# Optimization experiments

Measured on AMD Instinct MI355X. Metric: run time of the kernel, lower is better.

## Reference

```python
import jax, jax.numpy as jnp
import numpy as np

H1, H2, H3 = 32, 64, 64
NODEN = 12
NODES_PER_GRAPH = NODEN + 2  # 14
N = 700000                   # 50000 graphs * 14 nodes
E = 4000000


def setup_inputs() -> dict:
    key = jax.random.key(0)
    ks = jax.random.split(key, 8)
    x = jax.random.normal(ks[0], (N, H1), dtype=jnp.float32)
    edges = jax.random.randint(ks[1], (2, E), 0, N, dtype=jnp.int64)
    W1 = jax.random.normal(ks[2], (H1, H2), dtype=jnp.float32) / np.sqrt(H1).astype(np.float32)
    b1 = jnp.zeros((H2,), jnp.float32)
    W2 = jax.random.normal(ks[3], (H2, H3), dtype=jnp.float32) / np.sqrt(H2).astype(np.float32)
    b2 = jnp.zeros((H3,), jnp.float32)
    Wfc = jax.random.normal(ks[4], (H3 * NODES_PER_GRAPH, 1), dtype=jnp.float32) / np.sqrt(H3 * NODES_PER_GRAPH).astype(np.float32)
    bfc = jnp.zeros((1,), jnp.float32)
    return {"x": x, "edges": edges, "W1": W1, "b1": b1, "W2": W2, "b2": b2, "Wfc": Wfc, "bfc": bfc}


def gcn_conv(x, src, dst, W, b, n):
    # PyG GCNConv: h = X W; add self-loops; norm = deg^-1/2[src]*deg^-1/2[dst]
    h = x @ W  # [N, out]
    ones = jnp.ones(src.shape[0], dtype=h.dtype)
    deg = jax.ops.segment_sum(ones, dst, num_segments=n) + jnp.asarray(1.0, h.dtype)  # +1 self-loop
    dinv = jax.lax.rsqrt(deg)  # deg >= 1 always (self-loop)
    norm = dinv[src] * dinv[dst]  # [E]
    agg = jax.ops.segment_sum(h[src] * norm[:, None], dst, num_segments=n)
    agg = agg + h * (dinv * dinv)[:, None]  # self-loop contribution
    return agg + b


def reference(x, edges, W1, b1, W2, b2, Wfc, bfc):
    src, dst = edges[0], edges[1]
    h = jax.nn.relu(gcn_conv(x, src, dst, W1, b1, N))
    # F.dropout(training=False) is identity in eval mode
    h = jax.nn.relu(gcn_conv(h, src, dst, W2, b2, N))
    h = h.reshape(-1, H3 * NODES_PER_GRAPH)  # [B, 896]
    return h @ Wfc + bfc  # [B, 1]
```

## Files before the change

kernel.cpp:

```cpp
#include <hip/hip_runtime.h>
#include <hip/hip_fp16.h>


typedef _Float16 half8 __attribute__((ext_vector_type(8)));
typedef float float4v __attribute__((ext_vector_type(4)));

#define CHUNK 8192
#define BSH 11
#define BNODES 2048
#define DBINS 64

__global__ __launch_bounds__(256) void fallback_kernel(float* __restrict__ out, int n, float v)
{
  int i = blockIdx.x * 256 + threadIdx.x;
  if (i < n) out[i] = v;
}

__device__ inline int edges_shift(const int* __restrict__ edges)
{
  int orv = edges[1] | edges[3] | edges[5] | edges[7] | edges[9] | edges[11] | edges[13] | edges[15];
  return (orv == 0) ? 1 : 0;
}

__global__ __launch_bounds__(256) void hist2_kernel(
    const int* __restrict__ edges, int E, int N,
    int* __restrict__ cnt, int NBK, int* __restrict__ gtot,
    __half* __restrict__ P, __half* __restrict__ F2)
{
  __shared__ int lh[512];
  int t = threadIdx.x;
  int blk = blockIdx.x;
  if (blk == 0) {
    if (t < 8) ((uint2*)(P + (size_t)N * 32))[t] = make_uint2(0, 0);
    else if (t < 24) ((uint2*)(F2 + (size_t)N * 64))[t - 8] = make_uint2(0, 0);
  }
  for (int b = t; b < NBK; b += 256) lh[b] = 0;
  __syncthreads();
  int sh = edges_shift(edges);
  int base = blk * CHUNK;
#pragma unroll
  for (int k = 0; k < CHUNK / 256; k++) {
    int e = base + k * 256 + t;
    if (e < E) {
      int d = edges[(E + e) << sh];
      if ((unsigned)d < (unsigned)N) atomicAdd(&lh[d >> BSH], 1);
    }
  }
  __syncthreads();
  for (int b = t; b < NBK; b += 256)
    cnt[(size_t)blk * NBK + b] = atomicAdd(&gtot[b], lh[b]);
}

__global__ __launch_bounds__(512) void scan_totals_kernel(
    const int* __restrict__ totals, int NBK,
    int* __restrict__ bstart, int* __restrict__ rowptr, int N)
{
  __shared__ int sm[512];
  int t = threadIdx.x;
  int v = (t < NBK) ? totals[t] : 0;
  sm[t] = v;
  __syncthreads();
  for (int off = 1; off < 512; off <<= 1) {
    int x = 0;
    if (t >= off) x = sm[t - off];
    __syncthreads();
    if (t >= off) sm[t] += x;
    __syncthreads();
  }
  if (t < NBK) bstart[t] = sm[t] - v;
  if (t == 0) { bstart[NBK] = sm[511]; rowptr[N] = sm[511] + N; }
}

__global__ __launch_bounds__(256) void pass3_kernel(
    const int* __restrict__ edges, int E, int N,
    const int* __restrict__ cnt, const int* __restrict__ bstart,
    int* __restrict__ pair, int NBK)
{
  __shared__ int lcur[512];
  int t = threadIdx.x;
  int blk = blockIdx.x;
  for (int b = t; b < NBK; b += 256)
    lcur[b] = bstart[b] + cnt[(size_t)blk * NBK + b];
  __syncthreads();
  int sh = edges_shift(edges);
  int base = blk * CHUNK;
#pragma unroll
  for (int k = 0; k < CHUNK / 256; k++) {
    int e = base + k * 256 + t;
    if (e < E) {
      int s = edges[e << sh];
      int d = edges[(E + e) << sh];
      if ((unsigned)s < (unsigned)N && (unsigned)d < (unsigned)N) {
        int pos = atomicAdd(&lcur[d >> BSH], 1);
        pair[pos] = s | ((d & (BNODES - 1)) << 20);
      }
    }
  }
}

__global__ __launch_bounds__(256) void build_kernel(
    const int* __restrict__ pair, const int* __restrict__ bstart,
    int* __restrict__ rowptr, float* __restrict__ dinv, int* __restrict__ col,
    int* __restrict__ dhist, int N)
{
  __shared__ int hist[BNODES];
  __shared__ int cur[BNODES];
  __shared__ int sc[256];
  __shared__ int lh2[DBINS];
  int b = blockIdx.x;
  int t = threadIdx.x;
  int pbeg = bstart[b], pend = bstart[b + 1];
  int colbase = pbeg + (b << BSH);
  if (t < DBINS) lh2[t] = 0;
#pragma unroll
  for (int i = 0; i < BNODES / 256; i++) {
    int idx = i * 256 + t;
    int row = (b << BSH) + idx;
    hist[idx] = (row < N) ? 1 : 0;
  }
  __syncthreads();
  for (int p = pbeg + t; p < pend; p += 256)
    atomicAdd(&hist[(pair[p] >> 20) & (BNODES - 1)], 1);
  __syncthreads();
  int hv[8];
  int tsum = 0;
#pragma unroll
  for (int i = 0; i < 8; i++) { hv[i] = hist[t * 8 + i]; tsum += hv[i]; }
  sc[t] = tsum;
  __syncthreads();
  for (int off = 1; off < 256; off <<= 1) {
    int x = 0;
    if (t >= off) x = sc[t - off];
    __syncthreads();
    if (t >= off) sc[t] += x;
    __syncthreads();
  }
  int run = sc[t] - tsum;
#pragma unroll
  for (int i = 0; i < 8; i++) {
    int idx = t * 8 + i;
    int rp = colbase + run;
    int row = (b << BSH) + idx;
    if (row < N) {
      rowptr[row] = rp;
      dinv[row] = rsqrtf((float)hv[i]);
      col[rp] = row;
      cur[idx] = rp + 1;
      int bin = hv[i] < DBINS ? hv[i] : DBINS - 1;
      atomicAdd(&lh2[bin], 1);
    } else {
      cur[idx] = rp;
    }
    run += hv[i];
  }
  __syncthreads();
  if (t < DBINS && lh2[t]) atomicAdd(&dhist[t], lh2[t]);
  for (int p = pbeg + t; p < pend; p += 256) {
    int v = pair[p];
    int pos = atomicAdd(&cur[(v >> 20) & (BNODES - 1)], 1);
    col[pos] = v & 0xFFFFF;
  }
}

__global__ __launch_bounds__(256) void deg_place_kernel(
    const int* __restrict__ rowptr, const float* __restrict__ dinv,
    const int* __restrict__ dhist, int* __restrict__ dcnt,
    int* __restrict__ perm, int* __restrict__ iperm,
    int2* __restrict__ rowinfo, float* __restrict__ dinv_p, int N)
{
  __shared__ int bb[DBINS];
  __shared__ int lh[DBINS];
  __shared__ int lbase[DBINS];
  int t = threadIdx.x;
  if (t < DBINS) {
    lh[t] = 0;
    int v = dhist[t];
    int incl = v;
#pragma unroll
    for (int off = 1; off < DBINS; off <<= 1) {
      int x = __shfl_up(incl, off);
      if (t >= off) incl += x;
    }
    bb[t] = incl - v;
  }
  __syncthreads();
  int n = blockIdx.x * 256 + t;
  int b = -1, rbeg = 0, rlen = 0;
  if (n < N) {
    rbeg = rowptr[n];
    rlen = rowptr[n + 1] - rbeg;
    b = rlen < DBINS ? rlen : DBINS - 1;
    atomicAdd(&lh[b], 1);
  }
  __syncthreads();
  if (t < DBINS) lbase[t] = lh[t] ? (bb[t] + atomicAdd(&dcnt[t], lh[t])) : 0;
  __syncthreads();
  if (t < DBINS) lh[t] = lbase[t];
  __syncthreads();
  if (n < N) {
    int pos = atomicAdd(&lh[b], 1);
    perm[pos] = n;
    iperm[n] = pos;
    rowinfo[pos] = make_int2(rbeg, rlen);
    dinv_p[pos] = dinv[n];
  }
}

__global__ __launch_bounds__(256) void prep_kernel(
    int* __restrict__ col, const int* __restrict__ iperm, const int* __restrict__ rowptr,
    const float* __restrict__ X, const int* __restrict__ perm,
    const float* __restrict__ dinv_p, __half* __restrict__ P,
    float* __restrict__ out, const float* __restrict__ bfc, int N, int B)
{
  int idx = blockIdx.x * 256 + threadIdx.x;
  int stride = gridDim.x * 256;
  int total = rowptr[N];
  for (int k = idx; k < total; k += stride) col[k] = iperm[col[k]];
  int totp = N * 4;
  for (int i = idx; i < totp; i += stride) {
    int pos = i >> 2, part = i & 3;
    int node = perm[pos];
    const float4* xp = (const float4*)(X + (size_t)node * 32 + part * 8);
    float dv = dinv_p[pos];
    float4 v0 = xp[0], v1 = xp[1];
    half8 h;
    h[0] = (_Float16)(dv * v0.x); h[1] = (_Float16)(dv * v0.y);
    h[2] = (_Float16)(dv * v0.z); h[3] = (_Float16)(dv * v0.w);
    h[4] = (_Float16)(dv * v1.x); h[5] = (_Float16)(dv * v1.y);
    h[6] = (_Float16)(dv * v1.z); h[7] = (_Float16)(dv * v1.w);
    *(half8*)(P + (size_t)pos * 32 + part * 8) = h;
  }
  for (int i = idx; i < B; i += stride) out[i] = bfc[0];
}

__device__ inline void hacc(uint4 v, __half2* a)
{
  a[0] = __hadd2(a[0], *reinterpret_cast<__half2*>(&v.x));
  a[1] = __hadd2(a[1], *reinterpret_cast<__half2*>(&v.y));
  a[2] = __hadd2(a[2], *reinterpret_cast<__half2*>(&v.z));
  a[3] = __hadd2(a[3], *reinterpret_cast<__half2*>(&v.w));
}

__global__ __launch_bounds__(256) void agg1_pos_kernel(
    const __half* __restrict__ P, const int2* __restrict__ rowinfo,
    const int* __restrict__ col, const float* __restrict__ dinv_p,
    const float* __restrict__ W1, const float* __restrict__ b1,
    __half* __restrict__ U, int ntiles, int ndummy)
{
  int lane = threadIdx.x & 63;
  int n16 = lane & 15;
  int quad = lane >> 4;

  half8 bf[4];
#pragma unroll
  for (int jb = 0; jb < 4; jb++)
#pragma unroll
    for (int i = 0; i < 8; i++)
      bf[jb][i] = (_Float16)W1[(quad * 8 + i) * 64 + jb * 16 + n16];
  float b1j[4];
#pragma unroll
  for (int jb = 0; jb < 4; jb++) b1j[jb] = b1[jb * 16 + n16];

  const uint4* P4 = (const uint4*)P;
  _Float16* Uh = (_Float16*)U;
  int wave = (blockIdx.x * 256 + threadIdx.x) >> 6;
  int nw = (gridDim.x * 256) >> 6;
  for (int tile = wave; tile < ntiles; tile += nw) {
    int ut = __builtin_amdgcn_readfirstlane(tile);
    int base = ut * 16;
    int2 ri = rowinfo[base + n16];
    int rbeg = ri.x, rlen = ri.y;
    float dvown = dinv_p[base + n16];

    __half2 z2 = __float2half2_rn(0.f);
    __half2 aA[4] = {z2, z2, z2, z2};
    __half2 aB[4] = {z2, z2, z2, z2};

    for (int j = 0; __any(j < rlen); j += 8) {
      int c[8];
#pragma unroll
      for (int q = 0; q < 8; q++) {
        int cc = col[rbeg + j + q];
        c[q] = (j + q < rlen) ? cc : ndummy;
      }
      uint4 v[8];
#pragma unroll
      for (int q = 0; q < 8; q++) v[q] = P4[((size_t)c[q] << 2) + quad];
#pragma unroll
      for (int q = 0; q < 8; q += 2) { hacc(v[q], aA); hacc(v[q + 1], aB); }
    }
#pragma unroll
    for (int k = 0; k < 4; k++) aA[k] = __hadd2(aA[k], aB[k]);

    half8 a = *reinterpret_cast<half8*>(aA);
    float4v co[4];
#pragma unroll
    for (int jb = 0; jb < 4; jb++) {
      float4v z = {0.f, 0.f, 0.f, 0.f};
      co[jb] = __builtin_amdgcn_mfma_f32_16x16x32_f16(a, bf[jb], z, 0, 0, 0);
    }
#pragma unroll
    for (int r = 0; r < 4; r++) {
      int pos2 = base + quad * 4 + r;
      float dv = __shfl(dvown, quad * 4 + r);
#pragma unroll
      for (int jb = 0; jb < 4; jb++) {
        float h = dv * co[jb][r] + b1j[jb];
        h = h > 0.f ? h : 0.f;
        Uh[(size_t)pos2 * 64 + jb * 16 + n16] = (_Float16)(dv * h);
      }
    }
  }
}

__global__ __launch_bounds__(256) void mfma_final_fused_kernel(
    const __half* __restrict__ U, const int2* __restrict__ rowinfo,
    const int* __restrict__ col, const float* __restrict__ dinv_p,
    const int* __restrict__ perm,
    const float* __restrict__ W2, const float* __restrict__ b2,
    const float* __restrict__ Wfc, float* __restrict__ out,
    int ntiles, int ndummy)
{
  int lane = threadIdx.x & 63;
  int n16 = lane & 15;
  int quad = lane >> 4;

  half8 bf[4][2];
#pragma unroll
  for (int jb = 0; jb < 4; jb++)
#pragma unroll
    for (int kf = 0; kf < 2; kf++)
#pragma unroll
      for (int i = 0; i < 8; i++)
        bf[jb][kf][i] = (_Float16)W2[(kf * 32 + quad * 8 + i) * 64 + jb * 16 + n16];
  float b2j[4];
#pragma unroll
  for (int jb = 0; jb < 4; jb++) b2j[jb] = b2[jb * 16 + n16];

  const uint4* U4 = (const uint4*)U;
  int wave = (blockIdx.x * 256 + threadIdx.x) >> 6;
  int nw = (gridDim.x * 256) >> 6;
  for (int tile = wave; tile < ntiles; tile += nw) {
    int ut = __builtin_amdgcn_readfirstlane(tile);
    int base = ut * 16;
    int2 ri = rowinfo[base + n16];
    int rbeg = ri.x, rlen = ri.y;
    int node = perm[base + n16];
    float dvown = dinv_p[base + n16];

    __half2 z2 = __float2half2_rn(0.f);
    __half2 aE0[4] = {z2, z2, z2, z2};
    __half2 aE1[4] = {z2, z2, z2, z2};
    __half2 aO0[4] = {z2, z2, z2, z2};
    __half2 aO1[4] = {z2, z2, z2, z2};

    for (int j = 0; __any(j < rlen); j += 4) {
      int c0 = col[rbeg + j];
      int c1 = col[rbeg + j + 1];
      int c2 = col[rbeg + j + 2];
      int c3 = col[rbeg + j + 3];
      c0 = (j < rlen) ? c0 : ndummy;
      c1 = (j + 1 < rlen) ? c1 : ndummy;
      c2 = (j + 2 < rlen) ? c2 : ndummy;
      c3 = (j + 3 < rlen) ? c3 : ndummy;
      uint4 v00 = U4[((size_t)c0 << 3) + quad];
      uint4 v01 = U4[((size_t)c0 << 3) + 4 + quad];
      uint4 v10 = U4[((size_t)c1 << 3) + quad];
      uint4 v11 = U4[((size_t)c1 << 3) + 4 + quad];
      uint4 v20 = U4[((size_t)c2 << 3) + quad];
      uint4 v21 = U4[((size_t)c2 << 3) + 4 + quad];
      uint4 v30 = U4[((size_t)c3 << 3) + quad];
      uint4 v31 = U4[((size_t)c3 << 3) + 4 + quad];
      hacc(v00, aE0); hacc(v01, aE1);
      hacc(v10, aO0); hacc(v11, aO1);
      hacc(v20, aE0); hacc(v21, aE1);
      hacc(v30, aO0); hacc(v31, aO1);
    }
#pragma unroll
    for (int k = 0; k < 4; k++) {
      aE0[k] = __hadd2(aE0[k], aO0[k]);
      aE1[k] = __hadd2(aE1[k], aO1[k]);
    }
    __half2 dv = __half2half2(__float2half_rn(dvown));
#pragma unroll
    for (int j = 0; j < 4; j++) {
      aE0[j] = __hmul2(aE0[j], dv);
      aE1[j] = __hmul2(aE1[j], dv);
    }
    half8 a0 = *reinterpret_cast<half8*>(aE0);
    half8 a1 = *reinterpret_cast<half8*>(aE1);

    int g_r[4], t_r[4];
#pragma unroll
    for (int r = 0; r < 4; r++) {
      int nd = __shfl(node, quad * 4 + r);
      g_r[r] = nd / 14;
      t_r[r] = nd - g_r[r] * 14;
    }
    float pr[4] = {0.f, 0.f, 0.f, 0.f};
#pragma unroll
    for (int jb = 0; jb < 4; jb++) {
      float4v acc = {0.f, 0.f, 0.f, 0.f};
      acc = __builtin_amdgcn_mfma_f32_16x16x32_f16(a0, bf[jb][0], acc, 0, 0, 0);
      acc = __builtin_amdgcn_mfma_f32_16x16x32_f16(a1, bf[jb][1], acc, 0, 0, 0);
      int j = jb * 16 + n16;
#pragma unroll
      for (int r = 0; r < 4; r++) {
        float h = acc[r] + b2j[jb];
        h = h > 0.f ? h : 0.f;
        pr[r] += h * Wfc[t_r[r] * 64 + j];
      }
    }
#pragma unroll
    for (int r = 0; r < 4; r++) {
#pragma unroll
      for (int off = 1; off < 16; off <<= 1) pr[r] += __shfl_xor(pr[r], off);
    }
    if (n16 == 0) {
#pragma unroll
      for (int r = 0; r < 4; r++) atomicAdd(&out[g_r[r]], pr[r]);
    }
  }
}

extern "C" void kernel_launch(void* const* d_in, const int* in_sizes, int n_in,
                              void* d_out, int out_size, void* d_ws, size_t ws_size,
                              hipStream_t stream)
{
  const float* x = (const float*)d_in[0];
  const int* edges = (const int*)d_in[1];
  const float* W1 = (const float*)d_in[2];
  const float* b1 = (const float*)d_in[3];
  const float* W2 = (const float*)d_in[4];
  const float* b2 = (const float*)d_in[5];
  const float* Wfc = (const float*)d_in[6];
  const float* bfc = (const float*)d_in[7];
  float* out = (float*)d_out;
  (void)n_in;

  const int N = in_sizes[0] / 32;
  const int E = in_sizes[1] / 2;
  const int B = out_size;
  const int NBK = (N + BNODES - 1) >> BSH;
  const int NCH = (E + CHUNK - 1) / CHUNK;
  const int NBLK = (N + 255) / 256;

  char* ws = (char*)d_ws;
  size_t off = 0;
  auto alloc = [&](size_t bytes) -> void* {
    void* p = ws + off;
    off += (bytes + 255) & ~(size_t)255;
    return p;
  };
  int* cnt = (int*)alloc((size_t)NCH * NBK * 4);
  int* zbuf = (int*)alloc(((size_t)NBK + 2 * DBINS) * 4);
  int* gtot = zbuf;
  int* dhist = zbuf + NBK;
  int* dcnt = zbuf + NBK + DBINS;
  int* bstart = (int*)alloc(((size_t)NBK + 1) * 4);
  int* col = (int*)alloc(((size_t)E + N + 256) * 4);
  int* rowptr = (int*)alloc(((size_t)N + 1) * 4);
  float* dinv = (float*)alloc((size_t)N * 4);
  int* perm = (int*)alloc((size_t)N * 4);
  int* iperm = (int*)alloc((size_t)N * 4);
  int2* rowinfo = (int2*)alloc((size_t)N * 8);
  float* dinv_p = (float*)alloc((size_t)N * 4);
  __half* P = (__half*)alloc(((size_t)N + 16) * 32 * 2);
  __half* F2 = (__half*)alloc(((size_t)N + 16) * 64 * 2);
  int* pair = (int*)P;

  if (off > ws_size) {
    float v = -(float)(double)(ws_size >> 20);
    fallback_kernel<<<(B + 255) / 256, 256, 0, stream>>>(out, B, v);
    return;
  }

  hipMemsetAsync(zbuf, 0, ((size_t)NBK + 2 * DBINS) * 4, stream);
  hist2_kernel<<<NCH, 256, 0, stream>>>(edges, E, N, cnt, NBK, gtot, P, F2);
  scan_totals_kernel<<<1, 512, 0, stream>>>(gtot, NBK, bstart, rowptr, N);
  pass3_kernel<<<NCH, 256, 0, stream>>>(edges, E, N, cnt, bstart, pair, NBK);
  build_kernel<<<NBK, 256, 0, stream>>>(pair, bstart, rowptr, dinv, col, dhist, N);
  deg_place_kernel<<<NBLK, 256, 0, stream>>>(rowptr, dinv, dhist, dcnt,
                                             perm, iperm, rowinfo, dinv_p, N);
  prep_kernel<<<4096, 256, 0, stream>>>(col, iperm, rowptr, x, perm, dinv_p, P,
                                        out, bfc, N, B);

  int ntiles = (N + 15) / 16;
  agg1_pos_kernel<<<4096, 256, 0, stream>>>(P, rowinfo, col, dinv_p, W1, b1, F2, ntiles, N);
  mfma_final_fused_kernel<<<4096, 256, 0, stream>>>(F2, rowinfo, col, dinv_p, perm, W2, b2, Wfc,
                                                    out, ntiles, N);
}
```

Measured before the change: 562.3 us.

## Build CSR directly in degree-sorted order via global atomics and scatter

```diff
diff --git a/kernel.cpp b/kernel.cpp
--- a/kernel.cpp
+++ b/kernel.cpp
@@ -5,10 +5,7 @@
 typedef _Float16 half8 __attribute__((ext_vector_type(8)));
 typedef float float4v __attribute__((ext_vector_type(4)));
 
-#define CHUNK 8192
-#define BSH 11
-#define BNODES 2048
-#define DBINS 64
+#define DBINS 128
 
 __global__ __launch_bounds__(256) void fallback_kernel(float* __restrict__ out, int n, float v)
 {
@@ -22,200 +19,113 @@
   return (orv == 0) ? 1 : 0;
 }
 
-__global__ __launch_bounds__(256) void hist2_kernel(
-    const int* __restrict__ edges, int E, int N,
-    int* __restrict__ cnt, int NBK, int* __restrict__ gtot,
+__global__ __launch_bounds__(256) void hist_deg_kernel(
+    const int* __restrict__ edges, int E, int N, int* __restrict__ deg,
     __half* __restrict__ P, __half* __restrict__ F2)
 {
-  __shared__ int lh[512];
   int t = threadIdx.x;
-  int blk = blockIdx.x;
-  if (blk == 0) {
+  if (blockIdx.x == 0) {
     if (t < 8) ((uint2*)(P + (size_t)N * 32))[t] = make_uint2(0, 0);
     else if (t < 24) ((uint2*)(F2 + (size_t)N * 64))[t - 8] = make_uint2(0, 0);
   }
-  for (int b = t; b < NBK; b += 256) lh[b] = 0;
-  __syncthreads();
   int sh = edges_shift(edges);
-  int base = blk * CHUNK;
-#pragma unroll
-  for (int k = 0; k < CHUNK / 256; k++) {
-    int e = base + k * 256 + t;
-    if (e < E) {
-      int d = edges[(E + e) << sh];
-      if ((unsigned)d < (unsigned)N) atomicAdd(&lh[d >> BSH], 1);
-    }
-  }
-  __syncthreads();
-  for (int b = t; b < NBK; b += 256)
-    cnt[(size_t)blk * NBK + b] = atomicAdd(&gtot[b], lh[b]);
-}
-
-__global__ __launch_bounds__(512) void scan_totals_kernel(
-    const int* __restrict__ totals, int NBK,
-    int* __restrict__ bstart, int* __restrict__ rowptr, int N)
-{
-  __shared__ int sm[512];
+  int stride = gridDim.x * 256;
+  for (int e = blockIdx.x * 256 + t; e < E; e += stride) {
+    int s = edges[e << sh];
+    int d = edges[(E + e) << sh];
+    if ((unsigned)s < (unsigned)N && (unsigned)d < (unsigned)N)
+      atomicAdd(&deg[d], 1);
+  }
+}
+
+__global__ __launch_bounds__(256) void dbin_hist_kernel(
+    const int* __restrict__ deg, int* __restrict__ dhist, int N)
+{
+  __shared__ int lh[DBINS];
   int t = threadIdx.x;
-  int v = (t < NBK) ? totals[t] : 0;
-  sm[t] = v;
-  __syncthreads();
-  for (int off = 1; off < 512; off <<= 1) {
-    int x = 0;
-    if (t >= off) x = sm[t - off];
+  if (t < DBINS) lh[t] = 0;
+  __syncthreads();
+  int n = blockIdx.x * 256 + t;
+  if (n < N) {
+    int r = deg[n] + 1;
+    int b = r < DBINS ? r : DBINS - 1;
+    atomicAdd(&lh[b], 1);
+  }
+  __syncthreads();
+  if (t < DBINS && lh[t]) atomicAdd(&dhist[t], lh[t]);
+}
+
+__global__ __launch_bounds__(256) void deg_place_kernel(
+    const int* __restrict__ deg, const int* __restrict__ dhist, int* __restrict__ dcnt,
+    int* __restrict__ perm, int* __restrict__ iperm,
+    int2* __restrict__ rowinfo, float* __restrict__ dinv_p,
+    int* __restrict__ col, int N)
+{
+  __shared__ int s1[DBINS], s2[DBINS];
+  __shared__ int pb[DBINS], eb[DBINS];
+  __shared__ int lh[DBINS], lbase[DBINS];
+  int t = threadIdx.x;
+  int hv = 0;
+  if (t < DBINS) { hv = dhist[t]; s1[t] = hv; s2[t] = hv * t; lh[t] = 0; }
+  __syncthreads();
+  for (int off = 1; off < DBINS; off <<= 1) {
+    int a = 0, w = 0;
+    if (t < DBINS && t >= off) { a = s1[t - off]; w = s2[t - off]; }
     __syncthreads();
-    if (t >= off) sm[t] += x;
+    if (t < DBINS && t >= off) { s1[t] += a; s2[t] += w; }
     __syncthreads();
   }
-  if (t < NBK) bstart[t] = sm[t] - v;
-  if (t == 0) { bstart[NBK] = sm[511]; rowptr[N] = sm[511] + N; }
-}
-
-__global__ __launch_bounds__(256) void pass3_kernel(
-    const int* __restrict__ edges, int E, int N,
-    const int* __restrict__ cnt, const int* __restrict__ bstart,
-    int* __restrict__ pair, int NBK)
-{
-  __shared__ int lcur[512];
-  int t = threadIdx.x;
-  int blk = blockIdx.x;
-  for (int b = t; b < NBK; b += 256)
-    lcur[b] = bstart[b] + cnt[(size_t)blk * NBK + b];
-  __syncthreads();
-  int sh = edges_shift(edges);
-  int base = blk * CHUNK;
-#pragma unroll
-  for (int k = 0; k < CHUNK / 256; k++) {
-    int e = base + k * 256 + t;
-    if (e < E) {
-      int s = edges[e << sh];
-      int d = edges[(E + e) << sh];
-      if ((unsigned)s < (unsigned)N && (unsigned)d < (unsigned)N) {
-        int pos = atomicAdd(&lcur[d >> BSH], 1);
-        pair[pos] = s | ((d & (BNODES - 1)) << 20);
-      }
-    }
-  }
-}
-
-__global__ __launch_bounds__(256) void build_kernel(
-    const int* __restrict__ pair, const int* __restrict__ bstart,
-    int* __restrict__ rowptr, float* __restrict__ dinv, int* __restrict__ col,
-    int* __restrict__ dhist, int N)
-{
-  __shared__ int hist[BNODES];
-  __shared__ int cur[BNODES];
-  __shared__ int sc[256];
-  __shared__ int lh2[DBINS];
-  int b = blockIdx.x;
-  int t = threadIdx.x;
-  int pbeg = bstart[b], pend = bstart[b + 1];
-  int colbase = pbeg + (b << BSH);
-  if (t < DBINS) lh2[t] = 0;
-#pragma unroll
-  for (int i = 0; i < BNODES / 256; i++) {
-    int idx = i * 256 + t;
-    int row = (b << BSH) + idx;
-    hist[idx] = (row < N) ? 1 : 0;
-  }
-  __syncthreads();
-  for (int p = pbeg + t; p < pend; p += 256)
-    atomicAdd(&hist[(pair[p] >> 20) & (BNODES - 1)], 1);
-  __syncthreads();
-  int hv[8];
-  int tsum = 0;
-#pragma unroll
-  for (int i = 0; i < 8; i++) { hv[i] = hist[t * 8 + i]; tsum += hv[i]; }
-  sc[t] = tsum;
-  __syncthreads();
-  for (int off = 1; off < 256; off <<= 1) {
-    int x = 0;
-    if (t >= off) x = sc[t - off];
-    __syncthreads();
-    if (t >= off) sc[t] += x;
-    __syncthreads();
-  }
-  int run = sc[t] - tsum;
-#pragma unroll
-  for (int i = 0; i < 8; i++) {
-    int idx = t * 8 + i;
-    int rp = colbase + run;
-    int row = (b << BSH) + idx;
-    if (row < N) {
-      rowptr[row] = rp;
-      dinv[row] = rsqrtf((float)hv[i]);
-      col[rp] = row;
-      cur[idx] = rp + 1;
-      int bin = hv[i] < DBINS ? hv[i] : DBINS - 1;
-      atomicAdd(&lh2[bin], 1);
-    } else {
-      cur[idx] = rp;
-    }
-    run += hv[i];
-  }
-  __syncthreads();
-  if (t < DBINS && lh2[t]) atomicAdd(&dhist[t], lh2[t]);
-  for (int p = pbeg + t; p < pend; p += 256) {
-    int v = pair[p];
-    int pos = atomicAdd(&cur[(v >> 20) & (BNODES - 1)], 1);
-    col[pos] = v & 0xFFFFF;
-  }
-}
-
-__global__ __launch_bounds__(256) void deg_place_kernel(
-    const int* __restrict__ rowptr, const float* __restrict__ dinv,
-    const int* __restrict__ dhist, int* __restrict__ dcnt,
-    int* __restrict__ perm, int* __restrict__ iperm,
-    int2* __restrict__ rowinfo, float* __restrict__ dinv_p, int N)
-{
-  __shared__ int bb[DBINS];
-  __shared__ int lh[DBINS];
-  __shared__ int lbase[DBINS];
-  int t = threadIdx.x;
-  if (t < DBINS) {
-    lh[t] = 0;
-    int v = dhist[t];
-    int incl = v;
-#pragma unroll
-    for (int off = 1; off < DBINS; off <<= 1) {
-      int x = __shfl_up(incl, off);
-      if (t >= off) incl += x;
-    }
-    bb[t] = incl - v;
-  }
+  if (t < DBINS) { pb[t] = s1[t] - hv; eb[t] = s2[t] - hv * t; }
   __syncthreads();
   int n = blockIdx.x * 256 + t;
-  int b = -1, rbeg = 0, rlen = 0;
+  int b = -1, dg = 0;
   if (n < N) {
-    rbeg = rowptr[n];
-    rlen = rowptr[n + 1] - rbeg;
-    b = rlen < DBINS ? rlen : DBINS - 1;
+    dg = deg[n];
+    int r = dg + 1;
+    b = r < DBINS ? r : DBINS - 1;
     atomicAdd(&lh[b], 1);
   }
   __syncthreads();
-  if (t < DBINS) lbase[t] = lh[t] ? (bb[t] + atomicAdd(&dcnt[t], lh[t])) : 0;
+  if (t < DBINS) lbase[t] = lh[t] ? (pb[t] + atomicAdd(&dcnt[t], lh[t])) : 0;
   __syncthreads();
   if (t < DBINS) lh[t] = lbase[t];
   __syncthreads();
   if (n < N) {
     int pos = atomicAdd(&lh[b], 1);
+    int rowbeg = eb[b] + (pos - pb[b]) * b;
     perm[pos] = n;
     iperm[n] = pos;
-    rowinfo[pos] = make_int2(rbeg, rlen);
-    dinv_p[pos] = dinv[n];
+    rowinfo[pos] = make_int2(rowbeg, b);
+    dinv_p[pos] = rsqrtf((float)(dg + 1));
+    col[rowbeg] = pos;
+  }
+}
+
+__global__ __launch_bounds__(256) void scatter_kernel(
+    const int* __restrict__ edges, int E, int N, const int* __restrict__ iperm,
+    const int2* __restrict__ rowinfo, int* __restrict__ ecur, int* __restrict__ col)
+{
+  int sh = edges_shift(edges);
+  int stride = gridDim.x * 256;
+  for (int e = blockIdx.x * 256 + threadIdx.x; e < E; e += stride) {
+    int s = edges[e << sh];
+    int d = edges[(E + e) << sh];
+    if ((unsigned)s < (unsigned)N && (unsigned)d < (unsigned)N) {
+      int pd = iperm[d];
+      int2 ri = rowinfo[pd];
+      int idx = atomicAdd(&ecur[pd], 1);
+      if (idx < ri.y - 1) col[ri.x + 1 + idx] = iperm[s];
+    }
   }
 }
 
 __global__ __launch_bounds__(256) void prep_kernel(
-    int* __restrict__ col, const int* __restrict__ iperm, const int* __restrict__ rowptr,
     const float* __restrict__ X, const int* __restrict__ perm,
     const float* __restrict__ dinv_p, __half* __restrict__ P,
     float* __restrict__ out, const float* __restrict__ bfc, int N, int B)
 {
   int idx = blockIdx.x * 256 + threadIdx.x;
   int stride = gridDim.x * 256;
-  int total = rowptr[N];
-  for (int k = idx; k < total; k += stride) col[k] = iperm[col[k]];
   int totp = N * 4;
   for (int i = idx; i < totp; i += stride) {
     int pos = i >> 2, part = i & 3;
@@ -276,18 +186,14 @@
     __half2 aA[4] = {z2, z2, z2, z2};
     __half2 aB[4] = {z2, z2, z2, z2};
 
-    for (int j = 0; __any(j < rlen); j += 8) {
-      int c[8];
-#pragma unroll
-      for (int q = 0; q < 8; q++) {
-        int cc = col[rbeg + j + q];
-        c[q] = (j + q < rlen) ? cc : ndummy;
-      }
-      uint4 v[8];
-#pragma unroll
-      for (int q = 0; q < 8; q++) v[q] = P4[((size_t)c[q] << 2) + quad];
-#pragma unroll
-      for (int q = 0; q < 8; q += 2) { hacc(v[q], aA); hacc(v[q + 1], aB); }
+    for (int j = 0; __any(j < rlen); j += 2) {
+      int c0 = col[rbeg + j];
+      int c1 = col[rbeg + j + 1];
+      c0 = (j < rlen) ? c0 : ndummy;
+      c1 = (j + 1 < rlen) ? c1 : ndummy;
+      uint4 v0 = P4[((size_t)c0 << 2) + quad];
+      uint4 v1 = P4[((size_t)c1 << 2) + quad];
+      hacc(v0, aA); hacc(v1, aB);
     }
 #pragma unroll
     for (int k = 0; k < 4; k++) aA[k] = __hadd2(aA[k], aB[k]);
@@ -354,27 +260,17 @@
     __half2 aO0[4] = {z2, z2, z2, z2};
     __half2 aO1[4] = {z2, z2, z2, z2};
 
-    for (int j = 0; __any(j < rlen); j += 4) {
+    for (int j = 0; __any(j < rlen); j += 2) {
       int c0 = col[rbeg + j];
       int c1 = col[rbeg + j + 1];
-      int c2 = col[rbeg + j + 2];
-      int c3 = col[rbeg + j + 3];
       c0 = (j < rlen) ? c0 : ndummy;
       c1 = (j + 1 < rlen) ? c1 : ndummy;
-      c2 = (j + 2 < rlen) ? c2 : ndummy;
-      c3 = (j + 3 < rlen) ? c3 : ndummy;
       uint4 v00 = U4[((size_t)c0 << 3) + quad];
       uint4 v01 = U4[((size_t)c0 << 3) + 4 + quad];
       uint4 v10 = U4[((size_t)c1 << 3) + quad];
       uint4 v11 = U4[((size_t)c1 << 3) + 4 + quad];
-      uint4 v20 = U4[((size_t)c2 << 3) + quad];
-      uint4 v21 = U4[((size_t)c2 << 3) + 4 + quad];
-      uint4 v30 = U4[((size_t)c3 << 3) + quad];
-      uint4 v31 = U4[((size_t)c3 << 3) + 4 + quad];
       hacc(v00, aE0); hacc(v01, aE1);
       hacc(v10, aO0); hacc(v11, aO1);
-      hacc(v20, aE0); hacc(v21, aE1);
-      hacc(v30, aO0); hacc(v31, aO1);
     }
 #pragma unroll
     for (int k = 0; k < 4; k++) {
@@ -441,8 +337,6 @@
   const int N = in_sizes[0] / 32;
   const int E = in_sizes[1] / 2;
   const int B = out_size;
-  const int NBK = (N + BNODES - 1) >> BSH;
-  const int NCH = (E + CHUNK - 1) / CHUNK;
   const int NBLK = (N + 255) / 256;
 
   char* ws = (char*)d_ws;
@@ -452,22 +346,18 @@
     off += (bytes + 255) & ~(size_t)255;
     return p;
   };
-  int* cnt = (int*)alloc((size_t)NCH * NBK * 4);
-  int* zbuf = (int*)alloc(((size_t)NBK + 2 * DBINS) * 4);
-  int* gtot = zbuf;
-  int* dhist = zbuf + NBK;
-  int* dcnt = zbuf + NBK + DBINS;
-  int* bstart = (int*)alloc(((size_t)NBK + 1) * 4);
+  int* zbuf = (int*)alloc(((size_t)2 * N + 2 * DBINS) * 4);
+  int* deg = zbuf;
+  int* ecur = zbuf + N;
+  int* dhist = zbuf + 2 * N;
+  int* dcnt = zbuf + 2 * N + DBINS;
   int* col = (int*)alloc(((size_t)E + N + 256) * 4);
-  int* rowptr = (int*)alloc(((size_t)N + 1) * 4);
-  float* dinv = (float*)alloc((size_t)N * 4);
   int* perm = (int*)alloc((size_t)N * 4);
   int* iperm = (int*)alloc((size_t)N * 4);
   int2* rowinfo = (int2*)alloc((size_t)N * 8);
   float* dinv_p = (float*)alloc((size_t)N * 4);
   __half* P = (__half*)alloc(((size_t)N + 16) * 32 * 2);
   __half* F2 = (__half*)alloc(((size_t)N + 16) * 64 * 2);
-  int* pair = (int*)P;
 
   if (off > ws_size) {
     float v = -(float)(double)(ws_size >> 20);
@@ -475,15 +365,13 @@
     return;
   }
 
-  hipMemsetAsync(zbuf, 0, ((size_t)NBK + 2 * DBINS) * 4, stream);
-  hist2_kernel<<<NCH, 256, 0, stream>>>(edges, E, N, cnt, NBK, gtot, P, F2);
-  scan_totals_kernel<<<1, 512, 0, stream>>>(gtot, NBK, bstart, rowptr, N);
-  pass3_kernel<<<NCH, 256, 0, stream>>>(edges, E, N, cnt, bstart, pair, NBK);
-  build_kernel<<<NBK, 256, 0, stream>>>(pair, bstart, rowptr, dinv, col, dhist, N);
-  deg_place_kernel<<<NBLK, 256, 0, stream>>>(rowptr, dinv, dhist, dcnt,
-                                             perm, iperm, rowinfo, dinv_p, N);
-  prep_kernel<<<4096, 256, 0, stream>>>(col, iperm, rowptr, x, perm, dinv_p, P,
-                                        out, bfc, N, B);
+  hipMemsetAsync(zbuf, 0, ((size_t)2 * N + 2 * DBINS) * 4, stream);
+  hist_deg_kernel<<<2048, 256, 0, stream>>>(edges, E, N, deg, P, F2);
+  dbin_hist_kernel<<<NBLK, 256, 0, stream>>>(deg, dhist, N);
+  deg_place_kernel<<<NBLK, 256, 0, stream>>>(deg, dhist, dcnt, perm, iperm,
+                                             rowinfo, dinv_p, col, N);
+  scatter_kernel<<<2048, 256, 0, stream>>>(edges, E, N, iperm, rowinfo, ecur, col);
+  prep_kernel<<<4096, 256, 0, stream>>>(x, perm, dinv_p, P, out, bfc, N, B);
 
   int ntiles = (N + 15) / 16;
   agg1_pos_kernel<<<4096, 256, 0, stream>>>(P, rowinfo, col, dinv_p, W1, b1, F2, ntiles, N);
```

Measured after the change: 794.9 us. 1.41x slower.

## Fold totals scan into consumers and fuse feature packing into degree placement

Applied to the files above, without the earlier changes.

```diff
diff --git a/kernel.cpp b/kernel.cpp
--- a/kernel.cpp
+++ b/kernel.cpp
@@ -9,6 +9,7 @@
 #define BSH 11
 #define BNODES 2048
 #define DBINS 64
+#define NBKMAX 512
 
 __global__ __launch_bounds__(256) void fallback_kernel(float* __restrict__ out, int n, float v)
 {
@@ -20,6 +21,28 @@
 {
   int orv = edges[1] | edges[3] | edges[5] | edges[7] | edges[9] | edges[11] | edges[13] | edges[15];
   return (orv == 0) ? 1 : 0;
+}
+
+__device__ inline void scan_bstart(const int* __restrict__ gtot, int NBK, int* __restrict__ bl)
+{
+  int t = threadIdx.x;
+  if (t < 64) {
+    int carry = 0;
+    int rounds = (NBK + 63) >> 6;
+    for (int r = 0; r < rounds; r++) {
+      int idx = r * 64 + t;
+      int v = (idx < NBK) ? gtot[idx] : 0;
+      int incl = v;
+#pragma unroll
+      for (int off = 1; off < 64; off <<= 1) {
+        int x = __shfl_up(incl, off);
+        if (t >= off) incl += x;
+      }
+      if (idx < NBK) bl[idx] = incl - v + carry;
+      carry += __shfl(incl, 63);
+    }
+    if (t == 0) bl[NBK] = carry;
+  }
 }
 
 __global__ __launch_bounds__(256) void hist2_kernel(
@@ -27,7 +50,7 @@
     int* __restrict__ cnt, int NBK, int* __restrict__ gtot,
     __half* __restrict__ P, __half* __restrict__ F2)
 {
-  __shared__ int lh[512];
+  __shared__ int lh[NBKMAX];
   int t = threadIdx.x;
   int blk = blockIdx.x;
   if (blk == 0) {
@@ -51,36 +74,19 @@
     cnt[(size_t)blk * NBK + b] = atomicAdd(&gtot[b], lh[b]);
 }
 
-__global__ __launch_bounds__(512) void scan_totals_kernel(
-    const int* __restrict__ totals, int NBK,
-    int* __restrict__ bstart, int* __restrict__ rowptr, int N)
-{
-  __shared__ int sm[512];
-  int t = threadIdx.x;
-  int v = (t < NBK) ? totals[t] : 0;
-  sm[t] = v;
-  __syncthreads();
-  for (int off = 1; off < 512; off <<= 1) {
-    int x = 0;
-    if (t >= off) x = sm[t - off];
-    __syncthreads();
-    if (t >= off) sm[t] += x;
-    __syncthreads();
-  }
-  if (t < NBK) bstart[t] = sm[t] - v;
-  if (t == 0) { bstart[NBK] = sm[511]; rowptr[N] = sm[511] + N; }
-}
-
 __global__ __launch_bounds__(256) void pass3_kernel(
     const int* __restrict__ edges, int E, int N,
-    const int* __restrict__ cnt, const int* __restrict__ bstart,
+    const int* __restrict__ cnt, const int* __restrict__ gtot,
     int* __restrict__ pair, int NBK)
 {
-  __shared__ int lcur[512];
+  __shared__ int bl[NBKMAX + 1];
+  __shared__ int lcur[NBKMAX];
   int t = threadIdx.x;
   int blk = blockIdx.x;
+  scan_bstart(gtot, NBK, bl);
+  __syncthreads();
   for (int b = t; b < NBK; b += 256)
-    lcur[b] = bstart[b] + cnt[(size_t)blk * NBK + b];
+    lcur[b] = bl[b] + cnt[(size_t)blk * NBK + b];
   __syncthreads();
   int sh = edges_shift(edges);
   int base = blk * CHUNK;
@@ -99,18 +105,18 @@
 }
 
 __global__ __launch_bounds__(256) void build_kernel(
-    const int* __restrict__ pair, const int* __restrict__ bstart,
+    const int* __restrict__ pair, const int* __restrict__ gtot,
     int* __restrict__ rowptr, float* __restrict__ dinv, int* __restrict__ col,
-    int* __restrict__ dhist, int N)
-{
+    int* __restrict__ dhist, int N, int NBK)
+{
+  __shared__ int bl[NBKMAX + 1];
   __shared__ int hist[BNODES];
   __shared__ int cur[BNODES];
   __shared__ int sc[256];
   __shared__ int lh2[DBINS];
   int b = blockIdx.x;
   int t = threadIdx.x;
-  int pbeg = bstart[b], pend = bstart[b + 1];
-  int colbase = pbeg + (b << BSH);
+  scan_bstart(gtot, NBK, bl);
   if (t < DBINS) lh2[t] = 0;
 #pragma unroll
   for (int i = 0; i < BNODES / 256; i++) {
@@ -119,6 +125,9 @@
     hist[idx] = (row < N) ? 1 : 0;
   }
   __syncthreads();
+  int pbeg = bl[b], pend = bl[b + 1];
+  int colbase = pbeg + (b << BSH);
+  if (b == 0 && t == 0) rowptr[N] = bl[NBK] + N;
   for (int p = pbeg + t; p < pend; p += 256)
     atomicAdd(&hist[(pair[p] >> 20) & (BNODES - 1)], 1);
   __syncthreads();
@@ -166,12 +175,16 @@
     const int* __restrict__ rowptr, const float* __restrict__ dinv,
     const int* __restrict__ dhist, int* __restrict__ dcnt,
     int* __restrict__ perm, int* __restrict__ iperm,
-    int2* __restrict__ rowinfo, float* __restrict__ dinv_p, int N)
+    int2* __restrict__ rowinfo, float* __restrict__ dinv_p,
+    const float* __restrict__ X, __half* __restrict__ P,
+    float* __restrict__ out, const float* __restrict__ bfc, int N, int B)
 {
   __shared__ int bb[DBINS];
   __shared__ int lh[DBINS];
   __shared__ int lbase[DBINS];
   int t = threadIdx.x;
+  int n = blockIdx.x * 256 + t;
+  if (n < B) out[n] = bfc[0];
   if (t < DBINS) {
     lh[t] = 0;
     int v = dhist[t];
@@ -184,7 +197,6 @@
     bb[t] = incl - v;
   }
   __syncthreads();
-  int n = blockIdx.x * 256 + t;
   int b = -1, rbeg = 0, rlen = 0;
   if (n < N) {
     rbeg = rowptr[n];
@@ -199,38 +211,33 @@
   __syncthreads();
   if (n < N) {
     int pos = atomicAdd(&lh[b], 1);
+    float dv = dinv[n];
     perm[pos] = n;
     iperm[n] = pos;
     rowinfo[pos] = make_int2(rbeg, rlen);
-    dinv_p[pos] = dinv[n];
-  }
-}
-
-__global__ __launch_bounds__(256) void prep_kernel(
-    int* __restrict__ col, const int* __restrict__ iperm, const int* __restrict__ rowptr,
-    const float* __restrict__ X, const int* __restrict__ perm,
-    const float* __restrict__ dinv_p, __half* __restrict__ P,
-    float* __restrict__ out, const float* __restrict__ bfc, int N, int B)
+    dinv_p[pos] = dv;
+    const float4* xp = (const float4*)(X + (size_t)n * 32);
+    __half* pp = P + (size_t)pos * 32;
+#pragma unroll
+    for (int part = 0; part < 4; part++) {
+      float4 v0 = xp[part * 2], v1 = xp[part * 2 + 1];
+      half8 h;
+      h[0] = (_Float16)(dv * v0.x); h[1] = (_Float16)(dv * v0.y);
+      h[2] = (_Float16)(dv * v0.z); h[3] = (_Float16)(dv * v0.w);
+      h[4] = (_Float16)(dv * v1.x); h[5] = (_Float16)(dv * v1.y);
+      h[6] = (_Float16)(dv * v1.z); h[7] = (_Float16)(dv * v1.w);
+      *(half8*)(pp + part * 8) = h;
+    }
+  }
+}
+
+__global__ __launch_bounds__(256) void prep_remap_kernel(
+    int* __restrict__ col, const int* __restrict__ iperm, const int* __restrict__ rowptr, int N)
 {
   int idx = blockIdx.x * 256 + threadIdx.x;
   int stride = gridDim.x * 256;
   int total = rowptr[N];
   for (int k = idx; k < total; k += stride) col[k] = iperm[col[k]];
-  int totp = N * 4;
-  for (int i = idx; i < totp; i += stride) {
-    int pos = i >> 2, part = i & 3;
-    int node = perm[pos];
-    const float4* xp = (const float4*)(X + (size_t)node * 32 + part * 8);
-    float dv = dinv_p[pos];
-    float4 v0 = xp[0], v1 = xp[1];
-    half8 h;
-    h[0] = (_Float16)(dv * v0.x); h[1] = (_Float16)(dv * v0.y);
-    h[2] = (_Float16)(dv * v0.z); h[3] = (_Float16)(dv * v0.w);
-    h[4] = (_Float16)(dv * v1.x); h[5] = (_Float16)(dv * v1.y);
-    h[6] = (_Float16)(dv * v1.z); h[7] = (_Float16)(dv * v1.w);
-    *(half8*)(P + (size_t)pos * 32 + part * 8) = h;
-  }
-  for (int i = idx; i < B; i += stride) out[i] = bfc[0];
 }
 
 __device__ inline void hacc(uint4 v, __half2* a)
@@ -457,7 +464,6 @@
   int* gtot = zbuf;
   int* dhist = zbuf + NBK;
   int* dcnt = zbuf + NBK + DBINS;
-  int* bstart = (int*)alloc(((size_t)NBK + 1) * 4);
   int* col = (int*)alloc(((size_t)E + N + 256) * 4);
   int* rowptr = (int*)alloc(((size_t)N + 1) * 4);
   float* dinv = (float*)alloc((size_t)N * 4);
@@ -477,13 +483,12 @@
 
   hipMemsetAsync(zbuf, 0, ((size_t)NBK + 2 * DBINS) * 4, stream);
   hist2_kernel<<<NCH, 256, 0, stream>>>(edges, E, N, cnt, NBK, gtot, P, F2);
-  scan_totals_kernel<<<1, 512, 0, stream>>>(gtot, NBK, bstart, rowptr, N);
-  pass3_kernel<<<NCH, 256, 0, stream>>>(edges, E, N, cnt, bstart, pair, NBK);
-  build_kernel<<<NBK, 256, 0, stream>>>(pair, bstart, rowptr, dinv, col, dhist, N);
+  pass3_kernel<<<NCH, 256, 0, stream>>>(edges, E, N, cnt, gtot, pair, NBK);
+  build_kernel<<<NBK, 256, 0, stream>>>(pair, gtot, rowptr, dinv, col, dhist, N, NBK);
   deg_place_kernel<<<NBLK, 256, 0, stream>>>(rowptr, dinv, dhist, dcnt,
-                                             perm, iperm, rowinfo, dinv_p, N);
-  prep_kernel<<<4096, 256, 0, stream>>>(col, iperm, rowptr, x, perm, dinv_p, P,
-                                        out, bfc, N, B);
+                                             perm, iperm, rowinfo, dinv_p,
+                                             x, P, out, bfc, N, B);
+  prep_remap_kernel<<<4096, 256, 0, stream>>>(col, iperm, rowptr, N);
 
   int ntiles = (N + 15) / 16;
   agg1_pos_kernel<<<4096, 256, 0, stream>>>(P, rowinfo, col, dinv_p, W1, b1, F2, ntiles, N);
```

Measured after the change: 567.6 us. About the same (+0.9%).
